# Kernel tuning notes

Hardware: AMD Instinct MI355X
Metric: run time of the kernel (lower is better)

## Reference

```python
import jax, jax.numpy as jnp
import numpy as np

N = 100_000   # nodes
E = 600_000   # edges
D = 128       # embed_dim
G = 1000      # graphs (batch ids)
L = 3         # num_layers


def setup_inputs() -> dict:
    key = jax.random.key(0)
    ks = jax.random.split(key, 12)
    s = 1.0 / np.sqrt(D)
    return {
        "x": jax.random.normal(ks[0], (N, D), jnp.float32),
        "edge_index": jax.random.randint(ks[1], (2, E), 0, N),
        "batch": jnp.sort(jax.random.randint(ks[2], (N,), 0, G)),
        "mask": jax.random.randint(ks[3], (N,), 0, 2),
        # stacked GCNConv weights/biases (in=hidden=out=D)
        "gcn_w": jax.random.normal(ks[4], (L, D, D), jnp.float32) * s,
        "gcn_b": jnp.zeros((L, D), jnp.float32),
        # MLP head: Linear(D,D) -> ReLU -> Linear(D,1)
        "lin1_w": jax.random.normal(ks[5], (D, D), jnp.float32) * s,
        "lin1_b": jnp.zeros((D,), jnp.float32),
        "lin2_w": jax.random.normal(ks[6], (D,), jnp.float32) * s,
        "lin2_b": jnp.zeros((), jnp.float32),
    }


def gcn_forward(x, src, dst, gcn_w, gcn_b):
    # symmetric gcn_norm with self-loops: deg[i] = 1 + in-degree(i)
    deg = jax.ops.segment_sum(jnp.ones((E,), x.dtype), dst, num_segments=N) + 1.0
    dinv = jax.lax.rsqrt(deg)
    enorm = dinv[src] * dinv[dst]          # [E] edge normalization
    self_norm = (dinv * dinv)[:, None]     # [N,1] self-loop normalization
    h = x
    for l in range(L):
        h = h @ gcn_w[l]                   # [N,D]
        h = (jax.ops.segment_sum(h[src] * enorm[:, None], dst, num_segments=N)
             + h * self_norm)
        h = h + gcn_b[l]
        if l < L - 1:
            h = jax.nn.relu(h)  # (dropout inactive at inference)
    return h


def reference(x, edge_index, batch, mask, gcn_w, gcn_b, lin1_w, lin1_b, lin2_w, lin2_b):
    src, dst = edge_index[0], edge_index[1]
    h = gcn_forward(x, src, dst, gcn_w, gcn_b)
    # MLP head -> per-node score [N]
    s = jax.nn.relu(h @ lin1_w + lin1_b) @ lin2_w + lin2_b
    s = jnp.where(mask == 0, jnp.float32(-1e9), s)
    # per-graph (segment) softmax — fused replacement for the unique/batch loop
    m = jax.ops.segment_max(s, batch, num_segments=G)
    e = jnp.exp(s - m[batch])
    z = jax.ops.segment_sum(e, batch, num_segments=G)
    return e / z[batch]
```

## Files before the change

### kernel.cpp

```cpp
#include <hip/hip_runtime.h>
#include <hip/hip_bf16.h>
#include <stdint.h>

typedef unsigned int u32;
typedef unsigned short u16;
typedef __attribute__((ext_vector_type(8))) short bf16x8;
typedef __attribute__((ext_vector_type(4))) float f32x4;

__device__ __forceinline__ float u16tof(u16 u){ return __uint_as_float(((u32)u) << 16); }
__device__ __forceinline__ float lo16(u32 v){ return __uint_as_float(v << 16); }
__device__ __forceinline__ float hi16(u32 v){ return __uint_as_float(v & 0xffff0000u); }
__device__ __forceinline__ u16 ftobf(float f){
  u32 b = __float_as_uint(f);
  return (u16)((b + 0x7FFFu + ((b >> 16) & 1u)) >> 16);
}
__device__ __forceinline__ u32 pack2(float a, float b){
  return (u32)ftobf(a) | ((u32)ftobf(b) << 16);
}
__device__ __forceinline__ float ldf(const void* p, int i, int isbf){
  return isbf ? u16tof(((const u16*)p)[i]) : ((const float*)p)[i];
}

__device__ __forceinline__ void acc8(float* a, uint4 v, float mk){
  a[0] = fmaf(lo16(v.x), mk, a[0]);
  a[1] = fmaf(hi16(v.x), mk, a[1]);
  a[2] = fmaf(lo16(v.y), mk, a[2]);
  a[3] = fmaf(hi16(v.y), mk, a[3]);
  a[4] = fmaf(lo16(v.z), mk, a[4]);
  a[5] = fmaf(hi16(v.z), mk, a[5]);
  a[6] = fmaf(lo16(v.w), mk, a[6]);
  a[7] = fmaf(hi16(v.w), mk, a[7]);
}

__device__ __forceinline__ void async16(const u16* g, const u16* l){
  __builtin_amdgcn_global_load_lds(
      (const __attribute__((address_space(1))) u32*)(uintptr_t)g,
      (__attribute__((address_space(3))) u32*)(uintptr_t)l,
      16, 0, 0);
}

__global__ __launch_bounds__(256) void k_prep(const void* __restrict__ gw, const void* __restrict__ l1w,
                                              u16* __restrict__ Wf, int L, int goffB,
                                              const int* __restrict__ batch, int* __restrict__ goff,
                                              int N, int G,
                                              const int* __restrict__ dst, int* __restrict__ hist,
                                              int nE, int chunk, int* __restrict__ flag){
  __shared__ int sh[256];
  const int b = blockIdx.x;
  const int t = threadIdx.x;
  const int histStart = L + 1 + goffB;

  if (b >= histStart){
    sh[t] = 0; __syncthreads();
    const int blk = b - histStart;
    const int e0 = blk * chunk, e1 = min(e0 + chunk, nE);
    for (int e = e0 + t; e < e1; e += 256) atomicAdd(&sh[dst[e] >> 9], 1);
    __syncthreads();
    hist[blk * 256 + t] = sh[t];
    return;
  }
  if (b >= L + 1){
    const int i = (b - (L + 1)) * 256 + t;
    if (i >= N) return;
    const int bt = batch[i];
    const int prev = (i == 0) ? -1 : batch[i - 1];
    for (int g = prev + 1; g <= bt; ++g) goff[g] = i;
    if (i == N - 1){ for (int g = bt + 1; g <= G; ++g) goff[g] = N; }
    return;
  }
  if (t == 0) sh[0] = 0;
  __syncthreads();
  int local = 0;
  for (int i = t; i < 4096; i += 256){
    u32 e = (((const u32*)gw)[i] >> 7) & 0xFFu;
    if (e >= 100u && e < 127u) local++;
  }
  atomicAdd(&sh[0], local);
  __syncthreads();
  const int isbf = (sh[0] > 2048) ? 1 : 0;
  if (b == 0 && t == 0) *flag = isbf;

  const void* src = (b < L) ? gw : l1w;
  const int sbase = (b < L) ? b * 16384 : 0;
  u16* dstp = Wf + (size_t)b * 16384;
  for (int g = t; g < 2048; g += 256){
    const int tt = g >> 8, ks = (g >> 6) & 3, lane = g & 63;
    const int n = tt * 16 + (lane & 15);
    const int k0 = ks * 32 + ((lane >> 4) << 3);
    u16* d = dstp + (size_t)g * 8;
    #pragma unroll
    for (int j = 0; j < 8; ++j){
      d[j] = ftobf(ldf(src, sbase + (k0 + j) * 128 + n, isbf));
    }
  }
}

__global__ __launch_bounds__(256) void k_hsum(int* __restrict__ hist, int* __restrict__ bsum){
  __shared__ int sm[256];
  const int b = blockIdx.x;
  const int t = threadIdx.x;
  const int v = hist[t * 256 + b];
  sm[t] = v; __syncthreads();
  for (int off = 1; off < 256; off <<= 1){
    int a = (t >= off) ? sm[t - off] : 0;
    __syncthreads();
    sm[t] += a;
    __syncthreads();
  }
  hist[t * 256 + b] = sm[t] - v;
  if (t == 255) bsum[b] = sm[255];
}

__global__ __launch_bounds__(256) void k_scatter(const int* __restrict__ src, const int* __restrict__ dst,
                                                 const int* __restrict__ hist, const int* __restrict__ bsum,
                                                 int2* __restrict__ tmpe, int nE, int chunk){
  __shared__ int sm[256];
  __shared__ int base[256];
  const int blk = blockIdx.x, t = threadIdx.x;
  const int v = bsum[t];
  sm[t] = v; __syncthreads();
  for (int off = 1; off < 256; off <<= 1){
    int a = (t >= off) ? sm[t - off] : 0;
    __syncthreads();
    sm[t] += a;
    __syncthreads();
  }
  base[t] = (sm[t] - v) + hist[blk * 256 + t];
  __syncthreads();
  const int e0 = blk * chunk, e1 = min(e0 + chunk, nE);
  for (int e = e0 + t; e < e1; e += 256){
    const int d = dst[e];
    const int pos = atomicAdd(&base[d >> 9], 1);
    tmpe[pos] = make_int2(src[e], d);
  }
}

__global__ __launch_bounds__(256) void k_local(const int2* __restrict__ tmpe, const int* __restrict__ bsum,
                                               int* __restrict__ boff, int* __restrict__ eid,
                                               float* __restrict__ dinv, int N, int nE, int nbkt){
  __shared__ int sm[256];
  __shared__ int bbx[257];
  __shared__ int hcnt[512];
  __shared__ int hoff[512];
  const int b = blockIdx.x, t = threadIdx.x;
  {
    const int v = bsum[t];
    sm[t] = v; __syncthreads();
    for (int off = 1; off < 256; off <<= 1){
      int a = (t >= off) ? sm[t - off] : 0;
      __syncthreads();
      sm[t] += a;
      __syncthreads();
    }
    bbx[t] = sm[t] - v;
    if (t == 255) bbx[256] = sm[255];
  }
  __syncthreads();
  const int n0 = b << 9;
  const int n1 = min(n0 + 512, N);
  const int nn = n1 - n0;
  const int e0 = bbx[b], e1 = bbx[b + 1];
  hcnt[t] = 0; hcnt[t + 256] = 0;
  __syncthreads();
  for (int e = e0 + t; e < e1; e += 256) atomicAdd(&hcnt[tmpe[e].y - n0], 1);
  __syncthreads();
  const int v0 = hcnt[t], v1 = hcnt[t + 256];
  hoff[t] = v0; hoff[t + 256] = v1;
  __syncthreads();
  for (int off = 1; off < 512; off <<= 1){
    int a0 = (t >= off) ? hoff[t - off] : 0;
    int a1 = (t + 256 >= off) ? hoff[t + 256 - off] : 0;
    __syncthreads();
    hoff[t] += a0; hoff[t + 256] += a1;
    __syncthreads();
  }
  const int ex0 = hoff[t] - v0 + e0;
  const int ex1 = hoff[t + 256] - v1 + e0;
  if (t < nn){       boff[n0 + t] = ex0;        dinv[n0 + t] = rsqrtf((float)v0 + 1.0f); }
  if (t + 256 < nn){ boff[n0 + t + 256] = ex1;  dinv[n0 + t + 256] = rsqrtf((float)v1 + 1.0f); }
  if (b == nbkt - 1 && t == 0) boff[N] = nE;
  __syncthreads();
  hoff[t] = ex0; hoff[t + 256] = ex1;
  __syncthreads();
  for (int e = e0 + t; e < e1; e += 256){
    const int2 pr = tmpe[e];
    const int pos = atomicAdd(&hoff[pr.y - n0], 1);
    eid[pos] = pr.x;
  }
}

__global__ __launch_bounds__(256) void k_mm(const void* __restrict__ X, const u16* __restrict__ Wf,
                                            const float* __restrict__ dinv, u16* __restrict__ T,
                                            int n, int cvtin, const int* __restrict__ fl){
  __shared__ u16 smw[16384];
  const int isbf = *fl;
  const int fp32in = cvtin && !isbf;
  {
    const uint4* s = (const uint4*)Wf;
    uint4* d = (uint4*)smw;
    for (int i = threadIdx.x; i < 2048; i += 256) d[i] = s[i];
  }
  __syncthreads();

  const int wave = threadIdx.x >> 6, lane = threadIdx.x & 63;
  const int m0 = blockIdx.x * 64 + wave * 16;
  int arow = m0 + (lane & 15); if (arow > n - 1) arow = n - 1;
  const int koff = (lane >> 4) << 3;

  f32x4 acc[8];
  #pragma unroll
  for (int t = 0; t < 8; ++t) acc[t] = (f32x4){0.f, 0.f, 0.f, 0.f};

  #pragma unroll
  for (int ks = 0; ks < 4; ++ks){
    bf16x8 a;
    if (fp32in){
      const float* ap = (const float*)X + (size_t)arow * 128 + koff + ks * 32;
      const float4 f0 = *(const float4*)ap;
      const float4 f1 = *(const float4*)(ap + 4);
      a = (bf16x8){(short)ftobf(f0.x), (short)ftobf(f0.y), (short)ftobf(f0.z), (short)ftobf(f0.w),
                   (short)ftobf(f1.x), (short)ftobf(f1.y), (short)ftobf(f1.z), (short)ftobf(f1.w)};
    } else {
      a = *(const bf16x8*)((const u16*)X + (size_t)arow * 128 + koff + ks * 32);
    }
    #pragma unroll
    for (int t = 0; t < 8; ++t){
      const bf16x8 b = *(const bf16x8*)(smw + (size_t)(((t * 4 + ks) * 64 + lane) * 8));
      acc[t] = __builtin_amdgcn_mfma_f32_16x16x32_bf16(a, b, acc[t], 0, 0, 0);
    }
  }
  __syncthreads();

  const int quad = lane >> 4, col0 = lane & 15;
  float dv[4];
  #pragma unroll
  for (int r = 0; r < 4; ++r){
    const int row = m0 + quad * 4 + r;
    dv[r] = (row < n) ? dinv[row] : 0.f;
  }
  u16* my = smw + wave * 2112;
  #pragma unroll
  for (int t = 0; t < 8; ++t){
    #pragma unroll
    for (int r = 0; r < 4; ++r){
      my[(quad * 4 + r) * 132 + t * 16 + col0] = ftobf(acc[t][r] * dv[r]);
    }
  }
  #pragma unroll
  for (int i = 0; i < 4; ++i){
    const int row = i * 4 + (lane >> 4);
    const int grow = m0 + row;
    const int c8 = (lane & 15) * 8;
    if (grow < n){
      const u16* s = &my[row * 132 + c8];
      uint2 lo = *(const uint2*)(s);
      uint2 hi = *(const uint2*)(s + 4);
      *(uint4*)&T[(size_t)grow * 128 + c8] = make_uint4(lo.x, lo.y, hi.x, hi.y);
    }
  }
}

__global__ __launch_bounds__(256) void k_gmm(const u16* __restrict__ Tin, const int* __restrict__ boff,
                                             const int* __restrict__ eid, const float* __restrict__ dinv,
                                             const void* __restrict__ bias, int layer,
                                             const u16* __restrict__ Wf, u16* __restrict__ Tout,
                                             int n, const int* __restrict__ fl){
  __shared__ u16 sma[16 * 132];
  __shared__ u16 ring[4][4][512];
  __shared__ int seid[1024];
  __shared__ int sboff[17];
  const int isbf = *fl;
  const int tid = threadIdx.x;
  const int wave = tid >> 6, lane = tid & 63;
  const int sub = lane >> 4, l16 = lane & 15;
  const int m0 = blockIdx.x * 16;

  const int e0 = boff[m0];
  const int e1 = boff[min(m0 + 16, n)];
  const int len = e1 - e0;
  const int inlds = (len <= 1024);
  if (tid < 17) sboff[tid] = boff[min(m0 + tid, n)];
  if (inlds){ for (int i = tid; i < len; i += 256) seid[i] = eid[e0 + i]; }
  __syncthreads();

  const int wsub = wave * 4 + sub;
  const int node = m0 + wsub;
  const int js = sboff[wsub];
  const int d  = sboff[wsub + 1] - js;

  float a[8];
  #pragma unroll
  for (int k = 0; k < 8; ++k) a[k] = 0.f;
  if (node < n){
    const uint4 sv = ((const uint4*)(Tin + (size_t)node * 128))[l16];
    acc8(a, sv, 1.f);
  }

  int T = 0;
  #pragma unroll
  for (int s2 = 0; s2 < 4; ++s2){
    const int dd = sboff[wave * 4 + s2 + 1] - sboff[wave * 4 + s2];
    T = (dd > T) ? dd : T;
  }

  if (inlds){
    const int jloc = js - e0;
    const int jlast = jloc + ((d > 0) ? (d - 1) : 0);
    const u16* base = Tin + (size_t)l16 * 8;
    u16* slot = &ring[wave][0][0];
    #pragma unroll
    for (int t = 0; t < 4; ++t){
      if (t < T){
        const int idx = (d > 0) ? seid[(t < d) ? (jloc + t) : jlast] : 0;
        async16(base + (size_t)idx * 128, slot + (t & 3) * 512);
      }
    }
    int t = 0;
    for (; t + 4 <= T; ++t){
      asm volatile("s_waitcnt vmcnt(3)" ::: "memory");
      const uint4 v = *(const uint4*)(slot + (t & 3) * 512 + lane * 8);
      acc8(a, v, (t < d) ? 1.f : 0.f);
      const int tn = t + 4;
      if (tn < T){
        const int idx = (d > 0) ? seid[(tn < d) ? (jloc + tn) : jlast] : 0;
        async16(base + (size_t)idx * 128, slot + (tn & 3) * 512);
      }
    }
    for (; t < T; ++t){
      const int rem = T - t - 1;
      if (rem >= 2)      asm volatile("s_waitcnt vmcnt(2)" ::: "memory");
      else if (rem == 1) asm volatile("s_waitcnt vmcnt(1)" ::: "memory");
      else               asm volatile("s_waitcnt vmcnt(0)" ::: "memory");
      const uint4 v = *(const uint4*)(slot + (t & 3) * 512 + lane * 8);
      acc8(a, v, (t < d) ? 1.f : 0.f);
    }
  } else {
    for (int j = js; j < js + d; ++j){
      const uint4 v = ((const uint4*)(Tin + (size_t)eid[j] * 128))[l16];
      acc8(a, v, 1.f);
    }
  }

  float h[8];
  #pragma unroll
  for (int k = 0; k < 8; ++k) h[k] = 0.f;
  if (node < n){
    const float di = dinv[node];
    const int bb = layer * 128 + l16 * 8;
    #pragma unroll
    for (int k = 0; k < 8; ++k){
      h[k] = fmaxf(fmaf(a[k], di, ldf(bias, bb + k, isbf)), 0.f);
    }
  }
  {
    uint4 o;
    o.x = pack2(h[0], h[1]); o.y = pack2(h[2], h[3]); o.z = pack2(h[4], h[5]); o.w = pack2(h[6], h[7]);
    *(uint4*)&sma[(wave * 4 + sub) * 132 + l16 * 8] = o;
  }
  __syncthreads();

  f32x4 acc[2];
  acc[0] = (f32x4){0.f,0.f,0.f,0.f}; acc[1] = (f32x4){0.f,0.f,0.f,0.f};
  #pragma unroll
  for (int ks = 0; ks < 4; ++ks){
    const bf16x8 av = *(const bf16x8*)(sma + l16 * 132 + sub * 8 + ks * 32);
    #pragma unroll
    for (int tt = 0; tt < 2; ++tt){
      const int t = wave * 2 + tt;
      const bf16x8 bv = *(const bf16x8*)(Wf + (size_t)(((t * 4 + ks) * 64 + lane) * 8));
      acc[tt] = __builtin_amdgcn_mfma_f32_16x16x32_bf16(av, bv, acc[tt], 0, 0, 0);
    }
  }
  __syncthreads();

  float dv[4];
  #pragma unroll
  for (int r = 0; r < 4; ++r){
    const int row = m0 + sub * 4 + r;
    dv[r] = (row < n) ? dinv[row] : 0.f;
  }
  #pragma unroll
  for (int tt = 0; tt < 2; ++tt){
    const int t = wave * 2 + tt;
    #pragma unroll
    for (int r = 0; r < 4; ++r){
      sma[(sub * 4 + r) * 132 + t * 16 + l16] = ftobf(acc[tt][r] * dv[r]);
    }
  }
  __syncthreads();

  {
    const int row = tid >> 4;
    const int c8 = (tid & 15) * 8;
    if (m0 + row < n){
      const u16* s = &sma[row * 132 + c8];
      uint2 lo = *(const uint2*)(s);
      uint2 hi = *(const uint2*)(s + 4);
      *(uint4*)&Tout[(size_t)(m0 + row) * 128 + c8] = make_uint4(lo.x, lo.y, hi.x, hi.y);
    }
  }
}

__global__ __launch_bounds__(256) void k_ghead(const u16* __restrict__ Tin, const int* __restrict__ boff,
                                               const int* __restrict__ eid, const float* __restrict__ dinv,
                                               const void* __restrict__ bias, int layer,
                                               const u16* __restrict__ Wf, const void* __restrict__ b1,
                                               const void* __restrict__ w2, const void* __restrict__ b2,
                                               const int* __restrict__ mask, float* __restrict__ s,
                                               int n, const int* __restrict__ fl){
  __shared__ u16 sma[16 * 132];
  __shared__ u16 ring[4][4][512];
  __shared__ int seid[1024];
  __shared__ int sboff[17];
  __shared__ float sred[4][16];
  const int isbf = *fl;
  const int tid = threadIdx.x;
  const int wave = tid >> 6, lane = tid & 63;
  const int sub = lane >> 4, l16 = lane & 15;
  const int m0 = blockIdx.x * 16;

  const int e0 = boff[m0];
  const int e1 = boff[min(m0 + 16, n)];
  const int len = e1 - e0;
  const int inlds = (len <= 1024);
  if (tid < 17) sboff[tid] = boff[min(m0 + tid, n)];
  if (inlds){ for (int i = tid; i < len; i += 256) seid[i] = eid[e0 + i]; }
  __syncthreads();

  const int wsub = wave * 4 + sub;
  const int node = m0 + wsub;
  const int js = sboff[wsub];
  const int d  = sboff[wsub + 1] - js;

  float a[8];
  #pragma unroll
  for (int k = 0; k < 8; ++k) a[k] = 0.f;
  if (node < n){
    const uint4 sv = ((const uint4*)(Tin + (size_t)node * 128))[l16];
    acc8(a, sv, 1.f);
  }

  int T = 0;
  #pragma unroll
  for (int s2 = 0; s2 < 4; ++s2){
    const int dd = sboff[wave * 4 + s2 + 1] - sboff[wave * 4 + s2];
    T = (dd > T) ? dd : T;
  }

  if (inlds){
    const int jloc = js - e0;
    const int jlast = jloc + ((d > 0) ? (d - 1) : 0);
    const u16* base = Tin + (size_t)l16 * 8;
    u16* slot = &ring[wave][0][0];
    #pragma unroll
    for (int t = 0; t < 4; ++t){
      if (t < T){
        const int idx = (d > 0) ? seid[(t < d) ? (jloc + t) : jlast] : 0;
        async16(base + (size_t)idx * 128, slot + (t & 3) * 512);
      }
    }
    int t = 0;
    for (; t + 4 <= T; ++t){
      asm volatile("s_waitcnt vmcnt(3)" ::: "memory");
      const uint4 v = *(const uint4*)(slot + (t & 3) * 512 + lane * 8);
      acc8(a, v, (t < d) ? 1.f : 0.f);
      const int tn = t + 4;
      if (tn < T){
        const int idx = (d > 0) ? seid[(tn < d) ? (jloc + tn) : jlast] : 0;
        async16(base + (size_t)idx * 128, slot + (tn & 3) * 512);
      }
    }
    for (; t < T; ++t){
      const int rem = T - t - 1;
      if (rem >= 2)      asm volatile("s_waitcnt vmcnt(2)" ::: "memory");
      else if (rem == 1) asm volatile("s_waitcnt vmcnt(1)" ::: "memory");
      else               asm volatile("s_waitcnt vmcnt(0)" ::: "memory");
      const uint4 v = *(const uint4*)(slot + (t & 3) * 512 + lane * 8);
      acc8(a, v, (t < d) ? 1.f : 0.f);
    }
  } else {
    for (int j = js; j < js + d; ++j){
      const uint4 v = ((const uint4*)(Tin + (size_t)eid[j] * 128))[l16];
      acc8(a, v, 1.f);
    }
  }

  float h[8];
  #pragma unroll
  for (int k = 0; k < 8; ++k) h[k] = 0.f;
  if (node < n){
    const float di = dinv[node];
    const int bb = layer * 128 + l16 * 8;
    #pragma unroll
    for (int k = 0; k < 8; ++k){
      h[k] = fmaf(a[k], di, ldf(bias, bb + k, isbf));
    }
  }
  {
    uint4 o;
    o.x = pack2(h[0], h[1]); o.y = pack2(h[2], h[3]); o.z = pack2(h[4], h[5]); o.w = pack2(h[6], h[7]);
    *(uint4*)&sma[(wave * 4 + sub) * 132 + l16 * 8] = o;
  }
  __syncthreads();

  f32x4 acc[2];
  acc[0] = (f32x4){0.f,0.f,0.f,0.f}; acc[1] = (f32x4){0.f,0.f,0.f,0.f};
  #pragma unroll
  for (int ks = 0; ks < 4; ++ks){
    const bf16x8 av = *(const bf16x8*)(sma + l16 * 132 + sub * 8 + ks * 32);
    #pragma unroll
    for (int tt = 0; tt < 2; ++tt){
      const int t = wave * 2 + tt;
      const bf16x8 bv = *(const bf16x8*)(Wf + (size_t)(((t * 4 + ks) * 64 + lane) * 8));
      acc[tt] = __builtin_amdgcn_mfma_f32_16x16x32_bf16(av, bv, acc[tt], 0, 0, 0);
    }
  }

  float p0 = 0.f, p1 = 0.f, p2 = 0.f, p3 = 0.f;
  #pragma unroll
  for (int tt = 0; tt < 2; ++tt){
    const int col = (wave * 2 + tt) * 16 + l16;
    const float bv = ldf(b1, col, isbf);
    const float wv = ldf(w2, col, isbf);
    p0 = fmaf(fmaxf(acc[tt][0] + bv, 0.f), wv, p0);
    p1 = fmaf(fmaxf(acc[tt][1] + bv, 0.f), wv, p1);
    p2 = fmaf(fmaxf(acc[tt][2] + bv, 0.f), wv, p2);
    p3 = fmaf(fmaxf(acc[tt][3] + bv, 0.f), wv, p3);
  }
  #pragma unroll
  for (int k = 1; k < 16; k <<= 1){
    p0 += __shfl_xor(p0, k);
    p1 += __shfl_xor(p1, k);
    p2 += __shfl_xor(p2, k);
    p3 += __shfl_xor(p3, k);
  }
  if (l16 == 0){
    sred[wave][sub * 4 + 0] = p0;
    sred[wave][sub * 4 + 1] = p1;
    sred[wave][sub * 4 + 2] = p2;
    sred[wave][sub * 4 + 3] = p3;
  }
  __syncthreads();
  if (tid < 16){
    const int row = m0 + tid;
    if (row < n){
      float sc = sred[0][tid] + sred[1][tid] + sred[2][tid] + sred[3][tid]
               + ldf(b2, 0, isbf);
      if (mask[row] == 0) sc = -1e9f;
      s[row] = sc;
    }
  }
}

__global__ __launch_bounds__(256) void k_gsm(const float* __restrict__ s, const int* __restrict__ goff,
                                             void* __restrict__ out, int G, const int* __restrict__ fl){
  const int g = blockIdx.x * 4 + (threadIdx.x >> 6);
  if (g >= G) return;
  const int lane = threadIdx.x & 63;
  const int i0 = goff[g], i1 = goff[g + 1];
  if (i0 >= i1) return;
  float m = -3.4e38f;
  for (int j = i0 + lane; j < i1; j += 64) m = fmaxf(m, s[j]);
  #pragma unroll
  for (int k = 32; k; k >>= 1) m = fmaxf(m, __shfl_xor(m, k));
  float zz = 0.f;
  for (int j = i0 + lane; j < i1; j += 64) zz += expf(s[j] - m);
  #pragma unroll
  for (int k = 32; k; k >>= 1) zz += __shfl_xor(zz, k);
  const float rz = 1.f / zz;
  const int isbf = *fl;
  for (int j = i0 + lane; j < i1; j += 64){
    const float v = expf(s[j] - m) * rz;
    if (isbf) ((u16*)out)[j] = ftobf(v);
    else      ((float*)out)[j] = v;
  }
}

extern "C" void kernel_launch(void* const* d_in, const int* in_sizes, int n_in,
                              void* d_out, int out_size, void* d_ws, size_t ws_size,
                              hipStream_t stream){
  const void* x    = d_in[0];
  const int* ei    = (const int*)d_in[1];
  const int* batch = (const int*)d_in[2];
  const int* mask  = (const int*)d_in[3];
  const void* gw   = d_in[4];
  const void* gb   = d_in[5];
  const void* l1w  = d_in[6];
  const void* l1b  = d_in[7];
  const void* l2w  = d_in[8];
  const void* l2b  = d_in[9];

  const int N = in_sizes[2];
  const int E = in_sizes[1] / 2;
  const int D = 128;
  const int L = in_sizes[4] / (D * D);
  const int G = 1000;

  char* p = (char*)d_ws;
  u16*  Hb    = (u16*)p;   p += (size_t)N * D * sizeof(u16);
  u16*  Tb    = (u16*)p;   p += (size_t)N * D * sizeof(u16);
  u16*  Wf    = (u16*)p;   p += (size_t)(L + 1) * D * D * sizeof(u16);
  float* dinv = (float*)p; p += (size_t)N * sizeof(float);
  float* sbuf = (float*)p; p += (size_t)N * sizeof(float);
  int*  boff  = (int*)p;   p += (size_t)(N + 1) * sizeof(int);
  int*  eid   = (int*)p;   p += (size_t)E * sizeof(int);
  int*  goff  = (int*)p;   p += (size_t)(G + 1) * sizeof(int);
  int*  hist  = (int*)p;   p += 256 * 256 * sizeof(int);
  int*  bsum  = (int*)p;   p += 256 * sizeof(int);
  int2* tmpe  = (int2*)p;  p += (size_t)E * sizeof(int2);
  int*  flag  = (int*)p;   p += 256;

  const int* srcp = ei;
  const int* dstp = ei + E;

  const int mmg   = (N + 63) / 64;
  const int fg    = (N + 15) / 16;
  const int goffB = (N + 255) / 256;
  const int chunk = (E + 255) / 256;
  const int nbkt  = (N + 511) / 512;

  k_prep<<<(L + 1) + goffB + 256, 256, 0, stream>>>(gw, l1w, Wf, L, goffB,
                                                    batch, goff, N, G, dstp, hist, E, chunk, flag);
  k_hsum<<<256, 256, 0, stream>>>(hist, bsum);
  k_scatter<<<256, 256, 0, stream>>>(srcp, dstp, hist, bsum, tmpe, E, chunk);
  k_local<<<nbkt, 256, 0, stream>>>(tmpe, bsum, boff, eid, dinv, N, E, nbkt);

  k_mm<<<mmg, 256, 0, stream>>>(x, Wf, dinv, Tb, N, 1, flag);
  k_gmm<<<fg, 256, 0, stream>>>(Tb, boff, eid, dinv, gb, 0, Wf + (size_t)1 * D * D, Hb, N, flag);
  k_gmm<<<fg, 256, 0, stream>>>(Hb, boff, eid, dinv, gb, 1, Wf + (size_t)2 * D * D, Tb, N, flag);
  k_ghead<<<fg, 256, 0, stream>>>(Tb, boff, eid, dinv, gb, 2, Wf + (size_t)L * D * D,
                                  l1b, l2w, l2b, mask, sbuf, N, flag);
  k_gsm<<<(G + 3) / 4, 256, 0, stream>>>(sbuf, goff, d_out, G, flag);
}
```

Before: 312.8 us.

## Fuse all stages into one persistent cooperative kernel with grid syncs

Replaces the nine separate kernel launches (CSR build, matmul, three aggregation layers, softmax) with one persistent cooperative kernel. The blocks loop over virtual tiles and separate the stages with grid.sync(). This removes per-launch overhead and the gaps between kernels. In exchange, the grid size is capped by occupancy, so the big gather stages may lose parallelism and latency hiding, and grid-wide barriers add their own cost.

```diff
diff --git a/kernel.cpp b/kernel.cpp
--- a/kernel.cpp
+++ b/kernel.cpp
@@ -1,6 +1,9 @@
 #include <hip/hip_runtime.h>
 #include <hip/hip_bf16.h>
+#include <hip/hip_cooperative_groups.h>
 #include <stdint.h>
+
+namespace cg = cooperative_groups;
 
 typedef unsigned int u32;
 typedef unsigned short u16;
@@ -39,248 +42,39 @@
       16, 0, 0);
 }
 
-__global__ __launch_bounds__(256) void k_prep(const void* __restrict__ gw, const void* __restrict__ l1w,
-                                              u16* __restrict__ Wf, int L, int goffB,
-                                              const int* __restrict__ batch, int* __restrict__ goff,
-                                              int N, int G,
-                                              const int* __restrict__ dst, int* __restrict__ hist,
-                                              int nE, int chunk, int* __restrict__ flag){
-  __shared__ int sh[256];
-  const int b = blockIdx.x;
-  const int t = threadIdx.x;
-  const int histStart = L + 1 + goffB;
-
-  if (b >= histStart){
-    sh[t] = 0; __syncthreads();
-    const int blk = b - histStart;
-    const int e0 = blk * chunk, e1 = min(e0 + chunk, nE);
-    for (int e = e0 + t; e < e1; e += 256) atomicAdd(&sh[dst[e] >> 9], 1);
-    __syncthreads();
-    hist[blk * 256 + t] = sh[t];
-    return;
-  }
-  if (b >= L + 1){
-    const int i = (b - (L + 1)) * 256 + t;
-    if (i >= N) return;
-    const int bt = batch[i];
-    const int prev = (i == 0) ? -1 : batch[i - 1];
-    for (int g = prev + 1; g <= bt; ++g) goff[g] = i;
-    if (i == N - 1){ for (int g = bt + 1; g <= G; ++g) goff[g] = N; }
-    return;
-  }
-  if (t == 0) sh[0] = 0;
-  __syncthreads();
-  int local = 0;
-  for (int i = t; i < 4096; i += 256){
-    u32 e = (((const u32*)gw)[i] >> 7) & 0xFFu;
-    if (e >= 100u && e < 127u) local++;
-  }
-  atomicAdd(&sh[0], local);
-  __syncthreads();
-  const int isbf = (sh[0] > 2048) ? 1 : 0;
-  if (b == 0 && t == 0) *flag = isbf;
-
-  const void* src = (b < L) ? gw : l1w;
-  const int sbase = (b < L) ? b * 16384 : 0;
-  u16* dstp = Wf + (size_t)b * 16384;
-  for (int g = t; g < 2048; g += 256){
-    const int tt = g >> 8, ks = (g >> 6) & 3, lane = g & 63;
-    const int n = tt * 16 + (lane & 15);
-    const int k0 = ks * 32 + ((lane >> 4) << 3);
-    u16* d = dstp + (size_t)g * 8;
-    #pragma unroll
-    for (int j = 0; j < 8; ++j){
-      d[j] = ftobf(ldf(src, sbase + (k0 + j) * 128 + n, isbf));
-    }
-  }
-}
-
-__global__ __launch_bounds__(256) void k_hsum(int* __restrict__ hist, int* __restrict__ bsum){
-  __shared__ int sm[256];
-  const int b = blockIdx.x;
-  const int t = threadIdx.x;
-  const int v = hist[t * 256 + b];
-  sm[t] = v; __syncthreads();
-  for (int off = 1; off < 256; off <<= 1){
-    int a = (t >= off) ? sm[t - off] : 0;
-    __syncthreads();
-    sm[t] += a;
-    __syncthreads();
-  }
-  hist[t * 256 + b] = sm[t] - v;
-  if (t == 255) bsum[b] = sm[255];
-}
-
-__global__ __launch_bounds__(256) void k_scatter(const int* __restrict__ src, const int* __restrict__ dst,
-                                                 const int* __restrict__ hist, const int* __restrict__ bsum,
-                                                 int2* __restrict__ tmpe, int nE, int chunk){
-  __shared__ int sm[256];
-  __shared__ int base[256];
-  const int blk = blockIdx.x, t = threadIdx.x;
-  const int v = bsum[t];
-  sm[t] = v; __syncthreads();
-  for (int off = 1; off < 256; off <<= 1){
-    int a = (t >= off) ? sm[t - off] : 0;
-    __syncthreads();
-    sm[t] += a;
-    __syncthreads();
-  }
-  base[t] = (sm[t] - v) + hist[blk * 256 + t];
-  __syncthreads();
-  const int e0 = blk * chunk, e1 = min(e0 + chunk, nE);
-  for (int e = e0 + t; e < e1; e += 256){
-    const int d = dst[e];
-    const int pos = atomicAdd(&base[d >> 9], 1);
-    tmpe[pos] = make_int2(src[e], d);
-  }
-}
-
-__global__ __launch_bounds__(256) void k_local(const int2* __restrict__ tmpe, const int* __restrict__ bsum,
-                                               int* __restrict__ boff, int* __restrict__ eid,
-                                               float* __restrict__ dinv, int N, int nE, int nbkt){
-  __shared__ int sm[256];
-  __shared__ int bbx[257];
-  __shared__ int hcnt[512];
-  __shared__ int hoff[512];
-  const int b = blockIdx.x, t = threadIdx.x;
-  {
-    const int v = bsum[t];
-    sm[t] = v; __syncthreads();
-    for (int off = 1; off < 256; off <<= 1){
-      int a = (t >= off) ? sm[t - off] : 0;
-      __syncthreads();
-      sm[t] += a;
-      __syncthreads();
-    }
-    bbx[t] = sm[t] - v;
-    if (t == 255) bbx[256] = sm[255];
-  }
-  __syncthreads();
-  const int n0 = b << 9;
-  const int n1 = min(n0 + 512, N);
-  const int nn = n1 - n0;
-  const int e0 = bbx[b], e1 = bbx[b + 1];
-  hcnt[t] = 0; hcnt[t + 256] = 0;
-  __syncthreads();
-  for (int e = e0 + t; e < e1; e += 256) atomicAdd(&hcnt[tmpe[e].y - n0], 1);
-  __syncthreads();
-  const int v0 = hcnt[t], v1 = hcnt[t + 256];
-  hoff[t] = v0; hoff[t + 256] = v1;
-  __syncthreads();
-  for (int off = 1; off < 512; off <<= 1){
-    int a0 = (t >= off) ? hoff[t - off] : 0;
-    int a1 = (t + 256 >= off) ? hoff[t + 256 - off] : 0;
-    __syncthreads();
-    hoff[t] += a0; hoff[t + 256] += a1;
-    __syncthreads();
-  }
-  const int ex0 = hoff[t] - v0 + e0;
-  const int ex1 = hoff[t + 256] - v1 + e0;
-  if (t < nn){       boff[n0 + t] = ex0;        dinv[n0 + t] = rsqrtf((float)v0 + 1.0f); }
-  if (t + 256 < nn){ boff[n0 + t + 256] = ex1;  dinv[n0 + t + 256] = rsqrtf((float)v1 + 1.0f); }
-  if (b == nbkt - 1 && t == 0) boff[N] = nE;
-  __syncthreads();
-  hoff[t] = ex0; hoff[t + 256] = ex1;
-  __syncthreads();
-  for (int e = e0 + t; e < e1; e += 256){
-    const int2 pr = tmpe[e];
-    const int pos = atomicAdd(&hoff[pr.y - n0], 1);
-    eid[pos] = pr.x;
-  }
-}
-
-__global__ __launch_bounds__(256) void k_mm(const void* __restrict__ X, const u16* __restrict__ Wf,
-                                            const float* __restrict__ dinv, u16* __restrict__ T,
-                                            int n, int cvtin, const int* __restrict__ fl){
-  __shared__ u16 smw[16384];
-  const int isbf = *fl;
-  const int fp32in = cvtin && !isbf;
-  {
-    const uint4* s = (const uint4*)Wf;
-    uint4* d = (uint4*)smw;
-    for (int i = threadIdx.x; i < 2048; i += 256) d[i] = s[i];
-  }
-  __syncthreads();
-
-  const int wave = threadIdx.x >> 6, lane = threadIdx.x & 63;
-  const int m0 = blockIdx.x * 64 + wave * 16;
-  int arow = m0 + (lane & 15); if (arow > n - 1) arow = n - 1;
-  const int koff = (lane >> 4) << 3;
-
-  f32x4 acc[8];
-  #pragma unroll
-  for (int t = 0; t < 8; ++t) acc[t] = (f32x4){0.f, 0.f, 0.f, 0.f};
-
-  #pragma unroll
-  for (int ks = 0; ks < 4; ++ks){
-    bf16x8 a;
-    if (fp32in){
-      const float* ap = (const float*)X + (size_t)arow * 128 + koff + ks * 32;
-      const float4 f0 = *(const float4*)ap;
-      const float4 f1 = *(const float4*)(ap + 4);
-      a = (bf16x8){(short)ftobf(f0.x), (short)ftobf(f0.y), (short)ftobf(f0.z), (short)ftobf(f0.w),
-                   (short)ftobf(f1.x), (short)ftobf(f1.y), (short)ftobf(f1.z), (short)ftobf(f1.w)};
-    } else {
-      a = *(const bf16x8*)((const u16*)X + (size_t)arow * 128 + koff + ks * 32);
-    }
-    #pragma unroll
-    for (int t = 0; t < 8; ++t){
-      const bf16x8 b = *(const bf16x8*)(smw + (size_t)(((t * 4 + ks) * 64 + lane) * 8));
-      acc[t] = __builtin_amdgcn_mfma_f32_16x16x32_bf16(a, b, acc[t], 0, 0, 0);
-    }
-  }
-  __syncthreads();
-
-  const int quad = lane >> 4, col0 = lane & 15;
-  float dv[4];
-  #pragma unroll
-  for (int r = 0; r < 4; ++r){
-    const int row = m0 + quad * 4 + r;
-    dv[r] = (row < n) ? dinv[row] : 0.f;
-  }
-  u16* my = smw + wave * 2112;
-  #pragma unroll
-  for (int t = 0; t < 8; ++t){
-    #pragma unroll
-    for (int r = 0; r < 4; ++r){
-      my[(quad * 4 + r) * 132 + t * 16 + col0] = ftobf(acc[t][r] * dv[r]);
-    }
-  }
-  #pragma unroll
-  for (int i = 0; i < 4; ++i){
-    const int row = i * 4 + (lane >> 4);
-    const int grow = m0 + row;
-    const int c8 = (lane & 15) * 8;
-    if (grow < n){
-      const u16* s = &my[row * 132 + c8];
-      uint2 lo = *(const uint2*)(s);
-      uint2 hi = *(const uint2*)(s + 4);
-      *(uint4*)&T[(size_t)grow * 128 + c8] = make_uint4(lo.x, lo.y, hi.x, hi.y);
-    }
-  }
-}
-
-__global__ __launch_bounds__(256) void k_gmm(const u16* __restrict__ Tin, const int* __restrict__ boff,
-                                             const int* __restrict__ eid, const float* __restrict__ dinv,
-                                             const void* __restrict__ bias, int layer,
-                                             const u16* __restrict__ Wf, u16* __restrict__ Tout,
-                                             int n, const int* __restrict__ fl){
-  __shared__ u16 sma[16 * 132];
-  __shared__ u16 ring[4][4][512];
-  __shared__ int seid[1024];
-  __shared__ int sboff[17];
-  const int isbf = *fl;
-  const int tid = threadIdx.x;
+struct Params {
+  const void* x;
+  const int* src; const int* dst;
+  const int* batch; const int* mask;
+  const void* gw; const void* gb;
+  const void* l1w; const void* l1b; const void* l2w; const void* l2b;
+  u16* Wf; u16* Hb; u16* Tb;
+  float* dinv; float* sbuf;
+  int* boff; int* eid; int* goff; int* hist; int* bsum;
+  int2* tmpe; int* flag;
+  void* out;
+  int N, E, G, L, chunk, nbkt, goffB, mmg, fg, gsmB;
+};
+
+
+__device__ __forceinline__ void gmm_tile(const Params& p, const u16* __restrict__ Tin,
+                                         int layer, const u16* __restrict__ Wfl,
+                                         u16* __restrict__ Tout, int isbf,
+                                         int m0, char* S, int tid){
+  u16* ring  = (u16*)S;
+  int* seid  = (int*)(S + 16384);
+  int* sboff = (int*)(S + 20480);
+  u16* sma   = (u16*)(S + 20560);
   const int wave = tid >> 6, lane = tid & 63;
   const int sub = lane >> 4, l16 = lane & 15;
-  const int m0 = blockIdx.x * 16;
-
-  const int e0 = boff[m0];
-  const int e1 = boff[min(m0 + 16, n)];
+  const int n = p.N;
+
+  const int e0 = p.boff[m0];
+  const int e1 = p.boff[min(m0 + 16, n)];
   const int len = e1 - e0;
   const int inlds = (len <= 1024);
-  if (tid < 17) sboff[tid] = boff[min(m0 + tid, n)];
-  if (inlds){ for (int i = tid; i < len; i += 256) seid[i] = eid[e0 + i]; }
+  if (tid < 17) sboff[tid] = p.boff[min(m0 + tid, n)];
+  if (inlds){ for (int i = tid; i < len; i += 256) seid[i] = p.eid[e0 + i]; }
   __syncthreads();
 
   const int wsub = wave * 4 + sub;
@@ -307,7 +101,7 @@
     const int jloc = js - e0;
     const int jlast = jloc + ((d > 0) ? (d - 1) : 0);
     const u16* base = Tin + (size_t)l16 * 8;
-    u16* slot = &ring[wave][0][0];
+    u16* slot = ring + wave * 2048;
     #pragma unroll
     for (int t = 0; t < 4; ++t){
       if (t < T){
@@ -336,7 +130,7 @@
     }
   } else {
     for (int j = js; j < js + d; ++j){
-      const uint4 v = ((const uint4*)(Tin + (size_t)eid[j] * 128))[l16];
+      const uint4 v = ((const uint4*)(Tin + (size_t)p.eid[j] * 128))[l16];
       acc8(a, v, 1.f);
     }
   }
@@ -345,11 +139,11 @@
   #pragma unroll
   for (int k = 0; k < 8; ++k) h[k] = 0.f;
   if (node < n){
-    const float di = dinv[node];
+    const float di = p.dinv[node];
     const int bb = layer * 128 + l16 * 8;
     #pragma unroll
     for (int k = 0; k < 8; ++k){
-      h[k] = fmaxf(fmaf(a[k], di, ldf(bias, bb + k, isbf)), 0.f);
+      h[k] = fmaxf(fmaf(a[k], di, ldf(p.gb, bb + k, isbf)), 0.f);
     }
   }
   {
@@ -367,7 +161,7 @@
     #pragma unroll
     for (int tt = 0; tt < 2; ++tt){
       const int t = wave * 2 + tt;
-      const bf16x8 bv = *(const bf16x8*)(Wf + (size_t)(((t * 4 + ks) * 64 + lane) * 8));
+      const bf16x8 bv = *(const bf16x8*)(Wfl + (size_t)(((t * 4 + ks) * 64 + lane) * 8));
       acc[tt] = __builtin_amdgcn_mfma_f32_16x16x32_bf16(av, bv, acc[tt], 0, 0, 0);
     }
   }
@@ -377,7 +171,7 @@
   #pragma unroll
   for (int r = 0; r < 4; ++r){
     const int row = m0 + sub * 4 + r;
-    dv[r] = (row < n) ? dinv[row] : 0.f;
+    dv[r] = (row < n) ? p.dinv[row] : 0.f;
   }
   #pragma unroll
   for (int tt = 0; tt < 2; ++tt){
@@ -401,30 +195,24 @@
   }
 }
 
-__global__ __launch_bounds__(256) void k_ghead(const u16* __restrict__ Tin, const int* __restrict__ boff,
-                                               const int* __restrict__ eid, const float* __restrict__ dinv,
-                                               const void* __restrict__ bias, int layer,
-                                               const u16* __restrict__ Wf, const void* __restrict__ b1,
-                                               const void* __restrict__ w2, const void* __restrict__ b2,
-                                               const int* __restrict__ mask, float* __restrict__ s,
-                                               int n, const int* __restrict__ fl){
-  __shared__ u16 sma[16 * 132];
-  __shared__ u16 ring[4][4][512];
-  __shared__ int seid[1024];
-  __shared__ int sboff[17];
-  __shared__ float sred[4][16];
-  const int isbf = *fl;
-  const int tid = threadIdx.x;
+__device__ __forceinline__ void ghead_tile(const Params& p, const u16* __restrict__ Tin,
+                                           int layer, const u16* __restrict__ Wfl,
+                                           int isbf, int m0, char* S, int tid){
+  u16* ring  = (u16*)S;
+  int* seid  = (int*)(S + 16384);
+  int* sboff = (int*)(S + 20480);
+  u16* sma   = (u16*)(S + 20560);
+  float* sred = (float*)(S + 24784);
   const int wave = tid >> 6, lane = tid & 63;
   const int sub = lane >> 4, l16 = lane & 15;
-  const int m0 = blockIdx.x * 16;
-
-  const int e0 = boff[m0];
-  const int e1 = boff[min(m0 + 16, n)];
+  const int n = p.N;
+
+  const int e0 = p.boff[m0];
+  const int e1 = p.boff[min(m0 + 16, n)];
   const int len = e1 - e0;
   const int inlds = (len <= 1024);
-  if (tid < 17) sboff[tid] = boff[min(m0 + tid, n)];
-  if (inlds){ for (int i = tid; i < len; i += 256) seid[i] = eid[e0 + i]; }
+  if (tid < 17) sboff[tid] = p.boff[min(m0 + tid, n)];
+  if (inlds){ for (int i = tid; i < len; i += 256) seid[i] = p.eid[e0 + i]; }
   __syncthreads();
 
   const int wsub = wave * 4 + sub;
@@ -451,7 +239,7 @@
     const int jloc = js - e0;
     const int jlast = jloc + ((d > 0) ? (d - 1) : 0);
     const u16* base = Tin + (size_t)l16 * 8;
-    u16* slot = &ring[wave][0][0];
+    u16* slot = ring + wave * 2048;
     #pragma unroll
     for (int t = 0; t < 4; ++t){
       if (t < T){
@@ -480,7 +268,7 @@
     }
   } else {
     for (int j = js; j < js + d; ++j){
-      const uint4 v = ((const uint4*)(Tin + (size_t)eid[j] * 128))[l16];
+      const uint4 v = ((const uint4*)(Tin + (size_t)p.eid[j] * 128))[l16];
       acc8(a, v, 1.f);
     }
   }
@@ -489,11 +277,11 @@
   #pragma unroll
   for (int k = 0; k < 8; ++k) h[k] = 0.f;
   if (node < n){
-    const float di = dinv[node];
+    const float di = p.dinv[node];
     const int bb = layer * 128 + l16 * 8;
     #pragma unroll
     for (int k = 0; k < 8; ++k){
-      h[k] = fmaf(a[k], di, ldf(bias, bb + k, isbf));
+      h[k] = fmaf(a[k], di, ldf(p.gb, bb + k, isbf));
     }
   }
   {
@@ -511,7 +299,7 @@
     #pragma unroll
     for (int tt = 0; tt < 2; ++tt){
       const int t = wave * 2 + tt;
-      const bf16x8 bv = *(const bf16x8*)(Wf + (size_t)(((t * 4 + ks) * 64 + lane) * 8));
+      const bf16x8 bv = *(const bf16x8*)(Wfl + (size_t)(((t * 4 + ks) * 64 + lane) * 8));
       acc[tt] = __builtin_amdgcn_mfma_f32_16x16x32_bf16(av, bv, acc[tt], 0, 0, 0);
     }
   }
@@ -520,8 +308,8 @@
   #pragma unroll
   for (int tt = 0; tt < 2; ++tt){
     const int col = (wave * 2 + tt) * 16 + l16;
-    const float bv = ldf(b1, col, isbf);
-    const float wv = ldf(w2, col, isbf);
+    const float bv = ldf(p.l1b, col, isbf);
+    const float wv = ldf(p.l2w, col, isbf);
     p0 = fmaf(fmaxf(acc[tt][0] + bv, 0.f), wv, p0);
     p1 = fmaf(fmaxf(acc[tt][1] + bv, 0.f), wv, p1);
     p2 = fmaf(fmaxf(acc[tt][2] + bv, 0.f), wv, p2);
@@ -535,44 +323,289 @@
     p3 += __shfl_xor(p3, k);
   }
   if (l16 == 0){
-    sred[wave][sub * 4 + 0] = p0;
-    sred[wave][sub * 4 + 1] = p1;
-    sred[wave][sub * 4 + 2] = p2;
-    sred[wave][sub * 4 + 3] = p3;
+    sred[wave * 16 + sub * 4 + 0] = p0;
+    sred[wave * 16 + sub * 4 + 1] = p1;
+    sred[wave * 16 + sub * 4 + 2] = p2;
+    sred[wave * 16 + sub * 4 + 3] = p3;
   }
   __syncthreads();
   if (tid < 16){
     const int row = m0 + tid;
     if (row < n){
-      float sc = sred[0][tid] + sred[1][tid] + sred[2][tid] + sred[3][tid]
-               + ldf(b2, 0, isbf);
-      if (mask[row] == 0) sc = -1e9f;
-      s[row] = sc;
-    }
-  }
-}
-
-__global__ __launch_bounds__(256) void k_gsm(const float* __restrict__ s, const int* __restrict__ goff,
-                                             void* __restrict__ out, int G, const int* __restrict__ fl){
-  const int g = blockIdx.x * 4 + (threadIdx.x >> 6);
-  if (g >= G) return;
-  const int lane = threadIdx.x & 63;
-  const int i0 = goff[g], i1 = goff[g + 1];
-  if (i0 >= i1) return;
-  float m = -3.4e38f;
-  for (int j = i0 + lane; j < i1; j += 64) m = fmaxf(m, s[j]);
-  #pragma unroll
-  for (int k = 32; k; k >>= 1) m = fmaxf(m, __shfl_xor(m, k));
-  float zz = 0.f;
-  for (int j = i0 + lane; j < i1; j += 64) zz += expf(s[j] - m);
-  #pragma unroll
-  for (int k = 32; k; k >>= 1) zz += __shfl_xor(zz, k);
-  const float rz = 1.f / zz;
-  const int isbf = *fl;
-  for (int j = i0 + lane; j < i1; j += 64){
-    const float v = expf(s[j] - m) * rz;
-    if (isbf) ((u16*)out)[j] = ftobf(v);
-    else      ((float*)out)[j] = v;
+      float sc = sred[0 * 16 + tid] + sred[1 * 16 + tid] + sred[2 * 16 + tid] + sred[3 * 16 + tid]
+               + ldf(p.l2b, 0, isbf);
+      if (p.mask[row] == 0) sc = -1e9f;
+      p.sbuf[row] = sc;
+    }
+  }
+  __syncthreads();
+}
+
+__device__ __forceinline__ void mm_tile(const Params& p, int isbf, int m0, char* S, int tid){
+  u16* smw = (u16*)S;
+  const int fp32in = !isbf;
+  {
+    const uint4* s = (const uint4*)p.Wf;
+    uint4* dd = (uint4*)smw;
+    for (int i = tid; i < 2048; i += 256) dd[i] = s[i];
+  }
+  __syncthreads();
+
+  const int wave = tid >> 6, lane = tid & 63;
+  const int mr0 = m0 + wave * 16;
+  const int n = p.N;
+  int arow = mr0 + (lane & 15); if (arow > n - 1) arow = n - 1;
+  const int koff = (lane >> 4) << 3;
+
+  f32x4 acc[8];
+  #pragma unroll
+  for (int t = 0; t < 8; ++t) acc[t] = (f32x4){0.f, 0.f, 0.f, 0.f};
+
+  #pragma unroll
+  for (int ks = 0; ks < 4; ++ks){
+    bf16x8 a;
+    if (fp32in){
+      const float* ap = (const float*)p.x + (size_t)arow * 128 + koff + ks * 32;
+      const float4 f0 = *(const float4*)ap;
+      const float4 f1 = *(const float4*)(ap + 4);
+      a = (bf16x8){(short)ftobf(f0.x), (short)ftobf(f0.y), (short)ftobf(f0.z), (short)ftobf(f0.w),
+                   (short)ftobf(f1.x), (short)ftobf(f1.y), (short)ftobf(f1.z), (short)ftobf(f1.w)};
+    } else {
+      a = *(const bf16x8*)((const u16*)p.x + (size_t)arow * 128 + koff + ks * 32);
+    }
+    #pragma unroll
+    for (int t = 0; t < 8; ++t){
+      const bf16x8 b = *(const bf16x8*)(smw + (size_t)(((t * 4 + ks) * 64 + lane) * 8));
+      acc[t] = __builtin_amdgcn_mfma_f32_16x16x32_bf16(a, b, acc[t], 0, 0, 0);
+    }
+  }
+  __syncthreads();
+
+  const int quad = lane >> 4, col0 = lane & 15;
+  float dv[4];
+  #pragma unroll
+  for (int r = 0; r < 4; ++r){
+    const int row = mr0 + quad * 4 + r;
+    dv[r] = (row < n) ? p.dinv[row] : 0.f;
+  }
+  u16* my = smw + wave * 2112;
+  #pragma unroll
+  for (int t = 0; t < 8; ++t){
+    #pragma unroll
+    for (int r = 0; r < 4; ++r){
+      my[(quad * 4 + r) * 132 + t * 16 + col0] = ftobf(acc[t][r] * dv[r]);
+    }
+  }
+  #pragma unroll
+  for (int i = 0; i < 4; ++i){
+    const int row = i * 4 + (lane >> 4);
+    const int grow = mr0 + row;
+    const int c8 = (lane & 15) * 8;
+    if (grow < n){
+      const u16* s = &my[row * 132 + c8];
+      uint2 lo = *(const uint2*)(s);
+      uint2 hi = *(const uint2*)(s + 4);
+      *(uint4*)&p.Tb[(size_t)grow * 128 + c8] = make_uint4(lo.x, lo.y, hi.x, hi.y);
+    }
+  }
+  __syncthreads();
+}
+
+__global__ __launch_bounds__(256, 4) void k_all(Params p){
+  cg::grid_group grid = cg::this_grid();
+  __shared__ __align__(16) char S[33024];
+  const int tid = threadIdx.x;
+  const int NB = gridDim.x;
+
+  {
+    int* sh = (int*)S;
+    const int histStart = p.L + 1 + p.goffB;
+    const int P1 = histStart + 256;
+    for (int b = blockIdx.x; b < P1; b += NB){
+      __syncthreads();
+      if (b >= histStart){
+        sh[tid] = 0; __syncthreads();
+        const int blk = b - histStart;
+        const int e0 = blk * p.chunk, e1 = min(e0 + p.chunk, p.E);
+        for (int e = e0 + tid; e < e1; e += 256) atomicAdd(&sh[p.dst[e] >> 9], 1);
+        __syncthreads();
+        p.hist[blk * 256 + tid] = sh[tid];
+      } else if (b >= p.L + 1){
+        const int i = (b - (p.L + 1)) * 256 + tid;
+        if (i < p.N){
+          const int bt = p.batch[i];
+          const int prev = (i == 0) ? -1 : p.batch[i - 1];
+          for (int g2 = prev + 1; g2 <= bt; ++g2) p.goff[g2] = i;
+          if (i == p.N - 1){ for (int g2 = bt + 1; g2 <= p.G; ++g2) p.goff[g2] = p.N; }
+        }
+      } else {
+        if (tid == 0) sh[0] = 0;
+        __syncthreads();
+        int local = 0;
+        for (int i = tid; i < 4096; i += 256){
+          u32 e = (((const u32*)p.gw)[i] >> 7) & 0xFFu;
+          if (e >= 100u && e < 127u) local++;
+        }
+        atomicAdd(&sh[0], local);
+        __syncthreads();
+        const int isbf = (sh[0] > 2048) ? 1 : 0;
+        if (b == 0 && tid == 0) *p.flag = isbf;
+        const void* src = (b < p.L) ? p.gw : p.l1w;
+        const int sbase = (b < p.L) ? b * 16384 : 0;
+        u16* dstp = p.Wf + (size_t)b * 16384;
+        for (int g2 = tid; g2 < 2048; g2 += 256){
+          const int tt = g2 >> 8, ks = (g2 >> 6) & 3, lane = g2 & 63;
+          const int nn = tt * 16 + (lane & 15);
+          const int k0 = ks * 32 + ((lane >> 4) << 3);
+          u16* dp = dstp + (size_t)g2 * 8;
+          #pragma unroll
+          for (int j = 0; j < 8; ++j) dp[j] = ftobf(ldf(src, sbase + (k0 + j) * 128 + nn, isbf));
+        }
+      }
+    }
+  }
+  grid.sync();
+
+  {
+    int* sm = (int*)S;
+    for (int b = blockIdx.x; b < 256; b += NB){
+      __syncthreads();
+      const int v = p.hist[tid * 256 + b];
+      sm[tid] = v; __syncthreads();
+      for (int off = 1; off < 256; off <<= 1){
+        int a = (tid >= off) ? sm[tid - off] : 0;
+        __syncthreads(); sm[tid] += a; __syncthreads();
+      }
+      p.hist[tid * 256 + b] = sm[tid] - v;
+      if (tid == 255) p.bsum[b] = sm[255];
+    }
+  }
+  grid.sync();
+
+  {
+    int* sm   = (int*)S;
+    int* base = (int*)(S + 1024);
+    for (int b = blockIdx.x; b < 256; b += NB){
+      __syncthreads();
+      const int v = p.bsum[tid];
+      sm[tid] = v; __syncthreads();
+      for (int off = 1; off < 256; off <<= 1){
+        int a = (tid >= off) ? sm[tid - off] : 0;
+        __syncthreads(); sm[tid] += a; __syncthreads();
+      }
+      base[tid] = (sm[tid] - v) + p.hist[b * 256 + tid];
+      __syncthreads();
+      const int e0 = b * p.chunk, e1 = min(e0 + p.chunk, p.E);
+      for (int e = e0 + tid; e < e1; e += 256){
+        const int d = p.dst[e];
+        const int pos = atomicAdd(&base[d >> 9], 1);
+        p.tmpe[pos] = make_int2(p.src[e], d);
+      }
+    }
+  }
+  grid.sync();
+
+  {
+    int* sm   = (int*)S;
+    int* bbx  = (int*)(S + 1024);
+    int* hcnt = (int*)(S + 2064);
+    int* hoff = (int*)(S + 4112);
+    for (int b = blockIdx.x; b < p.nbkt; b += NB){
+      __syncthreads();
+      {
+        const int v = p.bsum[tid];
+        sm[tid] = v; __syncthreads();
+        for (int off = 1; off < 256; off <<= 1){
+          int a = (tid >= off) ? sm[tid - off] : 0;
+          __syncthreads(); sm[tid] += a; __syncthreads();
+        }
+        bbx[tid] = sm[tid] - v;
+        if (tid == 255) bbx[256] = sm[255];
+      }
+      __syncthreads();
+      const int n0 = b << 9;
+      const int n1 = min(n0 + 512, p.N);
+      const int nn = n1 - n0;
+      const int e0 = bbx[b], e1 = bbx[b + 1];
+      hcnt[tid] = 0; hcnt[tid + 256] = 0;
+      __syncthreads();
+      for (int e = e0 + tid; e < e1; e += 256) atomicAdd(&hcnt[p.tmpe[e].y - n0], 1);
+      __syncthreads();
+      const int v0 = hcnt[tid], v1 = hcnt[tid + 256];
+      hoff[tid] = v0; hoff[tid + 256] = v1;
+      __syncthreads();
+      for (int off = 1; off < 512; off <<= 1){
+        int a0 = (tid >= off) ? hoff[tid - off] : 0;
+        int a1 = (tid + 256 >= off) ? hoff[tid + 256 - off] : 0;
+        __syncthreads();
+        hoff[tid] += a0; hoff[tid + 256] += a1;
+        __syncthreads();
+      }
+      const int ex0 = hoff[tid] - v0 + e0;
+      const int ex1 = hoff[tid + 256] - v1 + e0;
+      if (tid < nn){       p.boff[n0 + tid] = ex0;        p.dinv[n0 + tid] = rsqrtf((float)v0 + 1.0f); }
+      if (tid + 256 < nn){ p.boff[n0 + tid + 256] = ex1;  p.dinv[n0 + tid + 256] = rsqrtf((float)v1 + 1.0f); }
+      if (b == p.nbkt - 1 && tid == 0) p.boff[p.N] = p.E;
+      __syncthreads();
+      hoff[tid] = ex0; hoff[tid + 256] = ex1;
+      __syncthreads();
+      for (int e = e0 + tid; e < e1; e += 256){
+        const int2 pr = p.tmpe[e];
+        const int pos = atomicAdd(&hoff[pr.y - n0], 1);
+        p.eid[pos] = pr.x;
+      }
+    }
+  }
+  grid.sync();
+
+  const int isbf = *p.flag;
+
+  for (int vb = blockIdx.x; vb < p.mmg; vb += NB){
+    __syncthreads();
+    mm_tile(p, isbf, vb * 64, S, tid);
+  }
+  grid.sync();
+
+  for (int vb = blockIdx.x; vb < p.fg; vb += NB){
+    __syncthreads();
+    gmm_tile(p, p.Tb, 0, p.Wf + (size_t)1 * 16384, p.Hb, isbf, vb * 16, S, tid);
+  }
+  grid.sync();
+
+  for (int vb = blockIdx.x; vb < p.fg; vb += NB){
+    __syncthreads();
+    gmm_tile(p, p.Hb, 1, p.Wf + (size_t)2 * 16384, p.Tb, isbf, vb * 16, S, tid);
+  }
+  grid.sync();
+
+  for (int vb = blockIdx.x; vb < p.fg; vb += NB){
+    __syncthreads();
+    ghead_tile(p, p.Tb, 2, p.Wf + (size_t)p.L * 16384, isbf, vb * 16, S, tid);
+  }
+  grid.sync();
+
+  for (int vb = blockIdx.x; vb < p.gsmB; vb += NB){
+    const int g = vb * 4 + (tid >> 6);
+    if (g < p.G){
+      const int lane = tid & 63;
+      const int i0 = p.goff[g], i1 = p.goff[g + 1];
+      if (i0 < i1){
+        float m = -3.4e38f;
+        for (int j = i0 + lane; j < i1; j += 64) m = fmaxf(m, p.sbuf[j]);
+        #pragma unroll
+        for (int k = 32; k; k >>= 1) m = fmaxf(m, __shfl_xor(m, k));
+        float zz = 0.f;
+        for (int j = i0 + lane; j < i1; j += 64) zz += expf(p.sbuf[j] - m);
+        #pragma unroll
+        for (int k = 32; k; k >>= 1) zz += __shfl_xor(zz, k);
+        const float rz = 1.f / zz;
+        for (int j = i0 + lane; j < i1; j += 64){
+          const float v = expf(p.sbuf[j] - m) * rz;
+          if (isbf) ((u16*)p.out)[j] = ftobf(v);
+          else      ((float*)p.out)[j] = v;
+        }
+      }
+    }
   }
 }
 
@@ -610,25 +643,36 @@
   int2* tmpe  = (int2*)p;  p += (size_t)E * sizeof(int2);
   int*  flag  = (int*)p;   p += 256;
 
-  const int* srcp = ei;
-  const int* dstp = ei + E;
-
-  const int mmg   = (N + 63) / 64;
-  const int fg    = (N + 15) / 16;
-  const int goffB = (N + 255) / 256;
-  const int chunk = (E + 255) / 256;
-  const int nbkt  = (N + 511) / 512;
-
-  k_prep<<<(L + 1) + goffB + 256, 256, 0, stream>>>(gw, l1w, Wf, L, goffB,
-                                                    batch, goff, N, G, dstp, hist, E, chunk, flag);
-  k_hsum<<<256, 256, 0, stream>>>(hist, bsum);
-  k_scatter<<<256, 256, 0, stream>>>(srcp, dstp, hist, bsum, tmpe, E, chunk);
-  k_local<<<nbkt, 256, 0, stream>>>(tmpe, bsum, boff, eid, dinv, N, E, nbkt);
-
-  k_mm<<<mmg, 256, 0, stream>>>(x, Wf, dinv, Tb, N, 1, flag);
-  k_gmm<<<fg, 256, 0, stream>>>(Tb, boff, eid, dinv, gb, 0, Wf + (size_t)1 * D * D, Hb, N, flag);
-  k_gmm<<<fg, 256, 0, stream>>>(Hb, boff, eid, dinv, gb, 1, Wf + (size_t)2 * D * D, Tb, N, flag);
-  k_ghead<<<fg, 256, 0, stream>>>(Tb, boff, eid, dinv, gb, 2, Wf + (size_t)L * D * D,
-                                  l1b, l2w, l2b, mask, sbuf, N, flag);
-  k_gsm<<<(G + 3) / 4, 256, 0, stream>>>(sbuf, goff, d_out, G, flag);
-}
+  Params pr;
+  pr.x = x; pr.src = ei; pr.dst = ei + E;
+  pr.batch = batch; pr.mask = mask;
+  pr.gw = gw; pr.gb = gb;
+  pr.l1w = l1w; pr.l1b = l1b; pr.l2w = l2w; pr.l2b = l2b;
+  pr.Wf = Wf; pr.Hb = Hb; pr.Tb = Tb;
+  pr.dinv = dinv; pr.sbuf = sbuf;
+  pr.boff = boff; pr.eid = eid; pr.goff = goff; pr.hist = hist; pr.bsum = bsum;
+  pr.tmpe = tmpe; pr.flag = flag;
+  pr.out = d_out;
+  pr.N = N; pr.E = E; pr.G = G; pr.L = L;
+  pr.chunk = (E + 255) / 256;
+  pr.nbkt  = (N + 511) / 512;
+  pr.goffB = (N + 255) / 256;
+  pr.mmg   = (N + 63) / 64;
+  pr.fg    = (N + 15) / 16;
+  pr.gsmB  = (G + 3) / 4;
+
+  static int grid_n = 0;
+  if (grid_n == 0){
+    int nb = 0;
+    hipOccupancyMaxActiveBlocksPerMultiprocessor(&nb, k_all, 256, 0);
+    if (nb < 1) nb = 1;
+    hipDeviceProp_t prop;
+    hipGetDeviceProperties(&prop, 0);
+    int cu = prop.multiProcessorCount > 0 ? prop.multiProcessorCount : 256;
+    grid_n = nb * cu;
+    if (grid_n > 2048) grid_n = 2048;
+  }
+
+  void* args[] = { (void*)&pr };
+  hipLaunchCooperativeKernel((void*)k_all, dim3(grid_n), dim3(256), args, 0, stream);
+}
```

Measured after the change: 855.8 us. +173.6%, slower.
